# Performance work log

Hardware: AMD Instinct MI355X
Metric: run time of the kernel (lower is better)

## Reference

```python
import math
import jax, jax.numpy as jnp
import numpy as np

N_EMBD = 768
N_HEAD = 12
BLOCK_SIZE = 1024
B, T, N_ENC = 8, 1024, 257
EPS = 1e-5


def _ln(x, g, b):
    m = jnp.mean(x, axis=-1, keepdims=True)
    v = jnp.var(x, axis=-1, keepdims=True)
    return (x - m) * jax.lax.rsqrt(v + EPS) * g + b


def _heads(t, n_head):
    B_, N_, C_ = t.shape
    return t.reshape(B_, N_, n_head, C_ // n_head).transpose(0, 2, 1, 3)  # [B,H,N,D]


def setup_inputs() -> dict:
    key = jax.random.key(0)
    ks = jax.random.split(key, 16)
    s = 0.02
    d, h4, dq = N_EMBD, 4 * N_EMBD, N_EMBD // 4
    inp = {
        'x': jax.random.normal(ks[0], (B, T, d), jnp.float32),
        'x_enc': jax.random.normal(ks[1], (B, N_ENC, d), jnp.float32),
        'ln1_g': jnp.ones((d,), jnp.float32), 'ln1_b': jnp.zeros((d,), jnp.float32),
        'ln2_g': jnp.ones((d,), jnp.float32), 'ln2_b': jnp.zeros((d,), jnp.float32),
        'ln3_g': jnp.ones((d,), jnp.float32), 'ln3_b': jnp.zeros((d,), jnp.float32),
        'attn_w': jax.random.normal(ks[2], (d, 3 * d), jnp.float32) * s,
        'attn_bias': jnp.zeros((3 * d,), jnp.float32),
        'attn_proj_w': jax.random.normal(ks[3], (d, d), jnp.float32) * s,
        'attn_proj_b': jnp.zeros((d,), jnp.float32),
        'img_w': jax.random.normal(ks[4], (d, 2 * d), jnp.float32) * s,
        'img_b': jnp.zeros((2 * d,), jnp.float32),
        'cap_w': jax.random.normal(ks[5], (d, d), jnp.float32) * s,
        'cap_b': jnp.zeros((d,), jnp.float32),
        'cross_proj_w': jax.random.normal(ks[6], (d, d), jnp.float32) * s,
        'cross_proj_b': jnp.zeros((d,), jnp.float32),
        'ad1_w': jax.random.normal(ks[7], (d, dq), jnp.float32) * s,
        'ad1_b': jnp.zeros((dq,), jnp.float32),
        'ad2_w': jax.random.normal(ks[8], (dq, d), jnp.float32) * s,
        'ad2_b': jnp.zeros((d,), jnp.float32),
        'fc_w': jax.random.normal(ks[9], (d, h4), jnp.float32) * s,
        'fc_b': jnp.zeros((h4,), jnp.float32),
        'mproj_w': jax.random.normal(ks[10], (h4, d), jnp.float32) * s,
        'mproj_b': jnp.zeros((d,), jnp.float32),
    }
    return inp


def _block(x, x_enc, ln1_g, ln1_b, ln2_g, ln2_b, ln3_g, ln3_b,
           attn_w, attn_bias, attn_proj_w, attn_proj_b,
           img_w, img_b, cap_w, cap_b, cross_proj_w, cross_proj_b,
           ad1_w, ad1_b, ad2_w, ad2_b, fc_w, fc_b, mproj_w, mproj_b):
    d, nh = N_EMBD, N_HEAD
    hd = d // nh
    scale = 1.0 / math.sqrt(hd)

    def adapter(h):
        return jax.nn.relu(h @ ad1_w + ad1_b) @ ad2_w + ad2_b

    # --- causal self-attention ---
    h = _ln(x, ln1_g, ln1_b)
    qkv = h @ attn_w + attn_bias
    q, k, v = jnp.split(qkv, 3, axis=2)
    q, k, v = _heads(q, nh), _heads(k, nh), _heads(v, nh)  # [B,H,T,hd]
    att = jnp.einsum('bhqd,bhkd->bhqk', q, k) * scale
    Tq = x.shape[1]
    causal = jnp.tril(jnp.ones((Tq, Tq), bool))
    att = jnp.where(causal, att, -jnp.inf)
    att = jax.nn.softmax(att, axis=-1)
    sa = jnp.einsum('bhqk,bhkd->bhqd', att, v).transpose(0, 2, 1, 3).reshape(x.shape)
    sa = sa @ attn_proj_w + attn_proj_b
    x = x + adapter(sa)

    # --- cross-attention (queries from x, keys/values from x_enc) ---
    hq = _ln(x, ln1_g, ln1_b)
    he = _ln(x_enc, ln3_g, ln3_b)
    kv = he @ img_w + img_b
    k2, v2 = jnp.split(kv, 2, axis=2)
    q2 = hq @ cap_w + cap_b
    q2, k2, v2 = _heads(q2, nh), _heads(k2, nh), _heads(v2, nh)
    catt = jax.nn.softmax(jnp.einsum('bhqd,bhkd->bhqk', q2, k2) * scale, axis=-1)
    ca = jnp.einsum('bhqk,bhkd->bhqd', catt, v2).transpose(0, 2, 1, 3).reshape(x.shape)
    ca = ca @ cross_proj_w + cross_proj_b
    x = x + adapter(ca)

    # --- MLP ---
    hm = _ln(x, ln2_g, ln2_b)
    m = jax.nn.gelu(hm @ fc_w + fc_b, approximate=True) @ mproj_w + mproj_b
    x = x + adapter(m)
    return x, x_enc


def reference(x, x_enc, ln1_g, ln1_b, ln2_g, ln2_b, ln3_g, ln3_b,
              attn_w, attn_bias, attn_proj_w, attn_proj_b,
              img_w, img_b, cap_w, cap_b, cross_proj_w, cross_proj_b,
              ad1_w, ad1_b, ad2_w, ad2_b, fc_w, fc_b, mproj_w, mproj_b):
    return _block(x, x_enc, ln1_g, ln1_b, ln2_g, ln2_b, ln3_g, ln3_b,
                  attn_w, attn_bias, attn_proj_w, attn_proj_b,
                  img_w, img_b, cap_w, cap_b, cross_proj_w, cross_proj_b,
                  ad1_w, ad1_b, ad2_w, ad2_b, fc_w, fc_b, mproj_w, mproj_b)
```

## Files before the change

### kernel.cpp

```cpp
#include <hip/hip_runtime.h>

typedef unsigned short u16;
typedef short bf16x8 __attribute__((ext_vector_type(8)));
typedef float f32x4 __attribute__((ext_vector_type(4)));
typedef unsigned short u16x4 __attribute__((ext_vector_type(4)));

__device__ __forceinline__ u16 f2bf(float f) {
  union { float f; unsigned u; } v; v.f = f;
  unsigned u = v.u;
  unsigned r = (u + 0x7FFFu + ((u >> 16) & 1u)) >> 16;
  return (u16)r;
}
__device__ __forceinline__ float bf2f(u16 h) {
  union { unsigned u; float f; } v; v.u = ((unsigned)h) << 16;
  return v.f;
}
__device__ __forceinline__ unsigned cvt_pk_bf16(float lo, float hi) {
  unsigned d;
  asm("v_cvt_pk_bf16_f32 %0, %1, %2" : "=v"(d) : "v"(lo), "v"(hi));
  return d;
}
__device__ __forceinline__ float gelu_f(float x) {
  const float c1 = -2.302585093f;
  const float c2 = -0.1029620967f;
  float t = __builtin_fmaf(x * x, c2, c1) * x;
  float e = exp2f(t);
  return x * __builtin_amdgcn_rcpf(e + 1.0f);
}

#define GLD_LDS16(gp, lp)                                             \
  __builtin_amdgcn_global_load_lds(                                   \
      (const __attribute__((address_space(1))) void*)(gp),            \
      (__attribute__((address_space(3))) void*)(lp), 16, 0, 0)

template<int OFF>
__device__ __forceinline__ u16x4 tr16(unsigned a) {
  u16x4 d;
  asm volatile("ds_read_b64_tr_b16 %0, %1 offset:%2" : "=&v"(d) : "v"(a), "n"(OFF));
  return d;
}
__device__ __forceinline__ bf16x8 pack8(u16x4 a, u16x4 b) {
  union { u16x4 p[2]; bf16x8 v; } u;
  u.p[0] = a; u.p[1] = b;
  return u.v;
}
__device__ __forceinline__ u16x4 pack4(unsigned w0, unsigned w1) {
  union { unsigned w[2]; u16x4 v; } u;
  u.w[0] = w0; u.w[1] = w1;
  return u.v;
}

struct TrBatch {
  const float* W[9];
  u16* Bt[9];
  int K[9], N[9], Kpad[9], Npad[9];
  int tstart[10];
};
__global__ __launch_bounds__(256)
void transpose_all(TrBatch tb) {
  __shared__ float tile[64][65];
  const int tid = blockIdx.x;
  int mi = 0;
  while (mi < 8 && tid >= tb.tstart[mi + 1]) ++mi;
  const int lt = tid - tb.tstart[mi];
  const int tx = tb.Npad[mi] >> 6;
  const int n0 = (lt % tx) * 64;
  const int k0 = (lt / tx) * 64;
  const float* W = tb.W[mi];
  u16* Bt = tb.Bt[mi];
  const int K = tb.K[mi], N = tb.N[mi], Kpad = tb.Kpad[mi];
  const int t = threadIdx.x;
  const int c = t & 63;
  const int rb = t >> 6;
#pragma unroll
  for (int i = 0; i < 16; ++i) {
    int r = i * 4 + rb;
    float v = 0.f;
    if (k0 + r < K && n0 + c < N) v = W[(size_t)(k0 + r) * N + n0 + c];
    tile[r][c] = v;
  }
  __syncthreads();
#pragma unroll
  for (int i = 0; i < 16; ++i) {
    int r = i * 4 + rb;
    Bt[(size_t)(n0 + r) * Kpad + k0 + c] = f2bf(tile[c][r]);
  }
}

__global__ __launch_bounds__(64)
void ln_kernel(const float* __restrict__ X, const float* __restrict__ G,
               const float* __restrict__ Bv, u16* __restrict__ O, int Mreal) {
  const int row = blockIdx.x;
  const int l = threadIdx.x;
  u16* op = O + (size_t)row * 768;
  if (row >= Mreal) {
    u16x4 z = {0, 0, 0, 0};
#pragma unroll
    for (int i = 0; i < 3; ++i) *(u16x4*)(op + (i * 64 + l) * 4) = z;
    return;
  }
  const float* xp = X + (size_t)row * 768;
  float v[12];
  float s = 0.f, s2 = 0.f;
#pragma unroll
  for (int i = 0; i < 3; ++i) {
    float4 t4 = *(const float4*)(xp + (i * 64 + l) * 4);
    v[i * 4 + 0] = t4.x; v[i * 4 + 1] = t4.y; v[i * 4 + 2] = t4.z; v[i * 4 + 3] = t4.w;
    s += t4.x + t4.y + t4.z + t4.w;
    s2 += t4.x * t4.x + t4.y * t4.y + t4.z * t4.z + t4.w * t4.w;
  }
#pragma unroll
  for (int off = 32; off > 0; off >>= 1) {
    s += __shfl_xor(s, off);
    s2 += __shfl_xor(s2, off);
  }
  const float mean = s * (1.0f / 768.0f);
  const float var = s2 * (1.0f / 768.0f) - mean * mean;
  const float rstd = rsqrtf(var + 1e-5f);
#pragma unroll
  for (int i = 0; i < 3; ++i) {
    int base = (i * 64 + l) * 4;
    float4 g4 = *(const float4*)(G + base);
    float4 b4 = *(const float4*)(Bv + base);
    u16x4 o4;
    o4[0] = f2bf((v[i * 4 + 0] - mean) * rstd * g4.x + b4.x);
    o4[1] = f2bf((v[i * 4 + 1] - mean) * rstd * g4.y + b4.y);
    o4[2] = f2bf((v[i * 4 + 2] - mean) * rstd * g4.z + b4.z);
    o4[3] = f2bf((v[i * 4 + 3] - mean) * rstd * g4.w + b4.w);
    *(u16x4*)(op + base) = o4;
  }
}

template<bool DOLN, bool RESID>
__global__ __launch_bounds__(64)
void resid_ln(const float* __restrict__ S, float* __restrict__ D,
              const u16* __restrict__ P,
              const float* __restrict__ G, const float* __restrict__ Bv,
              u16* __restrict__ O) {
  const int row = blockIdx.x;
  const int l = threadIdx.x;
  const float* sp = S + (size_t)row * 768;
  float* dp = D + (size_t)row * 768;
  float v[12];
  float s = 0.f, s2 = 0.f;
#pragma unroll
  for (int i = 0; i < 3; ++i) {
    const int base = (i * 64 + l) * 4;
    float4 t4 = *(const float4*)(sp + base);
    if (RESID) {
      u16x4 p4 = *(const u16x4*)(P + (size_t)row * 768 + base);
      t4.x += bf2f(p4[0]); t4.y += bf2f(p4[1]);
      t4.z += bf2f(p4[2]); t4.w += bf2f(p4[3]);
    }
    v[i * 4 + 0] = t4.x; v[i * 4 + 1] = t4.y; v[i * 4 + 2] = t4.z; v[i * 4 + 3] = t4.w;
    s += t4.x + t4.y + t4.z + t4.w;
    s2 += t4.x * t4.x + t4.y * t4.y + t4.z * t4.z + t4.w * t4.w;
    *(float4*)(dp + base) = t4;
  }
  if (DOLN) {
#pragma unroll
    for (int off = 32; off > 0; off >>= 1) {
      s += __shfl_xor(s, off);
      s2 += __shfl_xor(s2, off);
    }
    const float mean = s * (1.0f / 768.0f);
    const float var = s2 * (1.0f / 768.0f) - mean * mean;
    const float rstd = rsqrtf(var + 1e-5f);
    u16* op = O + (size_t)row * 768;
#pragma unroll
    for (int i = 0; i < 3; ++i) {
      int base = (i * 64 + l) * 4;
      float4 g4 = *(const float4*)(G + base);
      float4 b4 = *(const float4*)(Bv + base);
      u16x4 o4;
      o4[0] = f2bf((v[i * 4 + 0] - mean) * rstd * g4.x + b4.x);
      o4[1] = f2bf((v[i * 4 + 1] - mean) * rstd * g4.y + b4.y);
      o4[2] = f2bf((v[i * 4 + 2] - mean) * rstd * g4.z + b4.z);
      o4[3] = f2bf((v[i * 4 + 3] - mean) * rstd * g4.w + b4.w);
      *(u16x4*)(op + base) = o4;
    }
  }
}

template<int MODE>
__global__ void gemm_bt(const u16* __restrict__ A, const u16* __restrict__ Bt,
                        void* __restrict__ C, const float* __restrict__ bias,
                        int K, int ldc, int nbias) {
  __shared__ u16 As[2 * 128 * 32];
  __shared__ u16 Bs[2 * 128 * 32];
  const int t = threadIdx.x;
  const int lane = t & 63;
  const int wid = t >> 6;
  const int wm = (wid >> 1) * 64;
  const int wn = (wid & 1) * 64;
  const int tm = blockIdx.x * 128;
  const int tn = blockIdx.y * 128;

  f32x4 zero = {0.f, 0.f, 0.f, 0.f};
  f32x4 acc[4][4];
#pragma unroll
  for (int i = 0; i < 4; ++i)
#pragma unroll
    for (int j = 0; j < 4; ++j) acc[i][j] = zero;

  const int rowA = lane & 15;
  const int kb = (((lane >> 4) ^ ((rowA >> 1) & 3)) << 3);
  const int kTiles = K >> 6;
  for (int kt = 0; kt < kTiles; ++kt) {
    const int kk = kt << 6;
#pragma unroll
    for (int i = 0; i < 4; ++i) {
      const int c = i * 256 + t;
      const int r = (c >> 2) & 127;
      const int cc = ((c >> 9) << 5) + ((((c & 3) ^ ((r >> 1) & 3))) << 3);
      GLD_LDS16(A + (size_t)(tm + r) * K + kk + cc, As + c * 8);
      GLD_LDS16(Bt + (size_t)(tn + r) * K + kk + cc, Bs + c * 8);
    }
    __syncthreads();
#pragma unroll
    for (int ks = 0; ks < 2; ++ks) {
      bf16x8 af[4], bfr[4];
      const int base = ks * 4096;
#pragma unroll
      for (int i = 0; i < 4; ++i) {
        af[i] = *(const bf16x8*)(As + base + (wm + i * 16 + rowA) * 32 + kb);
        bfr[i] = *(const bf16x8*)(Bs + base + (wn + i * 16 + rowA) * 32 + kb);
      }
#pragma unroll
      for (int mi = 0; mi < 4; ++mi)
#pragma unroll
        for (int ni = 0; ni < 4; ++ni)
          acc[mi][ni] = __builtin_amdgcn_mfma_f32_16x16x32_bf16(af[mi], bfr[ni], acc[mi][ni], 0, 0, 0);
    }
    __syncthreads();
  }
  const int col0 = lane & 15;
  const int row0 = (lane >> 4) << 2;
#pragma unroll
  for (int mi = 0; mi < 4; ++mi) {
#pragma unroll
    for (int ni = 0; ni < 4; ++ni) {
      int col = tn + wn + ni * 16 + col0;
      float bb = (col < nbias) ? bias[col] : 0.f;
      float vv[4];
#pragma unroll
      for (int r = 0; r < 4; ++r) {
        float v = acc[mi][ni][r] + bb;
        if (MODE == 1) v = fmaxf(v, 0.f);
        else if (MODE == 2) v = gelu_f(v);
        vv[r] = v;
      }
      unsigned w0 = cvt_pk_bf16(vv[0], vv[1]);
      unsigned w1 = cvt_pk_bf16(vv[2], vv[3]);
      size_t row = (size_t)(tm + wm + mi * 16 + row0);
      u16* cp = (u16*)C + row * ldc + col;
      cp[0] = (u16)w0;
      cp[(size_t)ldc] = (u16)(w0 >> 16);
      cp[(size_t)ldc * 2] = (u16)w1;
      cp[(size_t)ldc * 3] = (u16)(w1 >> 16);
    }
  }
}

struct GemmJob {
  const u16* A; const u16* Bt; u16* C; const float* bias;
  int K, ldc, nbias, mblocks;
};
__global__ __launch_bounds__(256)
void gemm_bt_dual(GemmJob j0, GemmJob j1, int split) {
  __shared__ u16 As[2 * 128 * 32];
  __shared__ u16 Bs[2 * 128 * 32];
  const int bid = blockIdx.x;
  const GemmJob& J = (bid < split) ? j0 : j1;
  const int lb = (bid < split) ? bid : bid - split;
  const int tm = (lb % J.mblocks) * 128;
  const int tn = (lb / J.mblocks) * 128;
  const u16* A = J.A;
  const u16* Bt = J.Bt;
  const int K = J.K;

  const int t = threadIdx.x;
  const int lane = t & 63;
  const int wid = t >> 6;
  const int wm = (wid >> 1) * 64;
  const int wn = (wid & 1) * 64;

  f32x4 zero = {0.f, 0.f, 0.f, 0.f};
  f32x4 acc[4][4];
#pragma unroll
  for (int i = 0; i < 4; ++i)
#pragma unroll
    for (int j = 0; j < 4; ++j) acc[i][j] = zero;

  const int rowA = lane & 15;
  const int kb = (((lane >> 4) ^ ((rowA >> 1) & 3)) << 3);
  const int kTiles = K >> 6;
  for (int kt = 0; kt < kTiles; ++kt) {
    const int kk = kt << 6;
#pragma unroll
    for (int i = 0; i < 4; ++i) {
      const int c = i * 256 + t;
      const int r = (c >> 2) & 127;
      const int cc = ((c >> 9) << 5) + ((((c & 3) ^ ((r >> 1) & 3))) << 3);
      GLD_LDS16(A + (size_t)(tm + r) * K + kk + cc, As + c * 8);
      GLD_LDS16(Bt + (size_t)(tn + r) * K + kk + cc, Bs + c * 8);
    }
    __syncthreads();
#pragma unroll
    for (int ks = 0; ks < 2; ++ks) {
      bf16x8 af[4], bfr[4];
      const int base = ks * 4096;
#pragma unroll
      for (int i = 0; i < 4; ++i) {
        af[i] = *(const bf16x8*)(As + base + (wm + i * 16 + rowA) * 32 + kb);
        bfr[i] = *(const bf16x8*)(Bs + base + (wn + i * 16 + rowA) * 32 + kb);
      }
#pragma unroll
      for (int mi = 0; mi < 4; ++mi)
#pragma unroll
        for (int ni = 0; ni < 4; ++ni)
          acc[mi][ni] = __builtin_amdgcn_mfma_f32_16x16x32_bf16(af[mi], bfr[ni], acc[mi][ni], 0, 0, 0);
    }
    __syncthreads();
  }
  const int col0 = lane & 15;
  const int row0 = (lane >> 4) << 2;
#pragma unroll
  for (int mi = 0; mi < 4; ++mi) {
#pragma unroll
    for (int ni = 0; ni < 4; ++ni) {
      int col = tn + wn + ni * 16 + col0;
      float bb = (col < J.nbias) ? J.bias[col] : 0.f;
      unsigned w0 = cvt_pk_bf16(acc[mi][ni][0] + bb, acc[mi][ni][1] + bb);
      unsigned w1 = cvt_pk_bf16(acc[mi][ni][2] + bb, acc[mi][ni][3] + bb);
      size_t row = (size_t)(tm + wm + mi * 16 + row0);
      u16* cp = J.C + row * J.ldc + col;
      cp[0] = (u16)w0;
      cp[(size_t)J.ldc] = (u16)(w0 >> 16);
      cp[(size_t)J.ldc * 2] = (u16)w1;
      cp[(size_t)J.ldc * 3] = (u16)(w1 >> 16);
    }
  }
}

template<bool CAUSAL>
__global__ __launch_bounds__(256)
void attn_mfma(const u16* __restrict__ Q, const u16* __restrict__ Kp,
               const u16* __restrict__ Vp,
               u16* __restrict__ O0, u16* __restrict__ O1, float2* __restrict__ ML,
               int seqkv, int qrs, int krs,
               long long qBatch, long long kBatch,
               int qoff, int koff, int voff) {
  __shared__ __align__(16) u16 Ks[64 * 64];
  __shared__ __align__(16) u16 Vs[4096];
  __shared__ __align__(16) u16 Ps[4][1024];
  const int t = threadIdx.x;
  const int lane = t & 63;
  const int wid = t >> 6;
  const int b = blockIdx.x / 12, h = blockIdx.x % 12;
  const int yq = CAUSAL ? ((int)gridDim.y - 1 - (int)blockIdx.y) : (int)blockIdx.y;
  const int q0 = yq * 64;
  const int colid = lane & 15;
  const int rgrp = lane >> 4;
  const int z = CAUSAL ? blockIdx.z : 0;

  int kt_begin = 0, kt_end;
  if (CAUSAL) {
    const int ntr = yq + 1;
    const int half = (ntr + 1) >> 1;
    kt_begin = z ? half : 0;
    kt_end = z ? ntr : half;
  } else {
    kt_end = (seqkv + 63) >> 6;
  }
  u16* Op = (CAUSAL && z) ? O1 : O0;

  if (CAUSAL && kt_begin >= kt_end) {
    if (colid == 0) {
#pragma unroll
      for (int r = 0; r < 4; ++r) {
        int qrow = q0 + wid * 16 + rgrp * 4 + r;
        ML[((size_t)z * 8192 + b * 1024 + qrow) * 12 + h] = make_float2(-1e30f, 0.f);
      }
    }
    return;
  }

  const u16* qp = Q + (size_t)b * qBatch + qoff + (size_t)(q0 + wid * 16 + colid) * qrs + h * 64;
  bf16x8 qa[2];
#pragma unroll
  for (int s = 0; s < 2; ++s) qa[s] = *(const bf16x8*)(qp + s * 32 + (rgrp << 3));

  f32x4 oacc[4];
#pragma unroll
  for (int i = 0; i < 4; ++i) oacc[i] = (f32x4){0.f, 0.f, 0.f, 0.f};
  float m[4] = {-1e30f, -1e30f, -1e30f, -1e30f};
  float l[4] = {0.f, 0.f, 0.f, 0.f};

  const u16* kbase = Kp + (size_t)b * kBatch + koff + h * 64;
  const u16* vbase = Vp + (size_t)b * kBatch + voff + h * 64;

  const int srr = t >> 3, sdc = t & 7;
  int kwo[2], vwo[2];
#pragma unroll
  for (int i = 0; i < 2; ++i) {
    const int r = srr + 32 * i;
    kwo[i] = r * 64 + ((sdc ^ (r & 7)) << 3);
    vwo[i] = ((sdc >> 1) << 10) + (i << 9) + (((srr >> 2) & 1) << 8)
           + (((srr >> 3) & 3) << 6) + ((srr & 3) << 4) + (((2 * sdc) & 3) << 2);
  }
  const unsigned vs_base = (unsigned)(size_t)&Vs[0] + 8u * (unsigned)lane;
  const unsigned ps_base = (unsigned)(size_t)&Ps[wid][0] + 8u * (unsigned)lane;

  bf16x8 kz[2], vz[2];
  auto LOADT = [&](int kt) {
    const int k0 = kt * 64;
#pragma unroll
    for (int i = 0; i < 2; ++i) {
      const int tk = k0 + srr + 32 * i;
      const int dc = sdc << 3;
      kz[i] = (bf16x8){0, 0, 0, 0, 0, 0, 0, 0};
      vz[i] = (bf16x8){0, 0, 0, 0, 0, 0, 0, 0};
      if (tk < seqkv) {
        kz[i] = *(const bf16x8*)(kbase + (size_t)tk * krs + dc);
        vz[i] = *(const bf16x8*)(vbase + (size_t)tk * krs + dc);
      }
    }
  };
  LOADT(kt_begin);

  constexpr float SC2 = 0.18033688011112042f;

  for (int kt = kt_begin; kt < kt_end; ++kt) {
    const int k0 = kt * 64;
#pragma unroll
    for (int i = 0; i < 2; ++i) {
      *(bf16x8*)&Ks[kwo[i]] = kz[i];
      *(bf16x8*)&Vs[vwo[i]] = vz[i];
    }
    __syncthreads();
    if (kt + 1 < kt_end) LOADT(kt + 1);

    f32x4 sacc[4];
#pragma unroll
    for (int c = 0; c < 4; ++c) sacc[c] = (f32x4){0.f, 0.f, 0.f, 0.f};
#pragma unroll
    for (int c = 0; c < 4; ++c)
#pragma unroll
      for (int s = 0; s < 2; ++s) {
        bf16x8 kf = *(const bf16x8*)&Ks[(c * 16 + colid) * 64 +
                                        ((((s << 2) + rgrp) ^ (colid & 7)) << 3)];
        sacc[c] = __builtin_amdgcn_mfma_f32_16x16x32_bf16(qa[s], kf, sacc[c], 0, 0, 0);
      }

    const bool domask = CAUSAL ? (kt == yq) : (kt == kt_end - 1);
    if (domask) {
#pragma unroll
      for (int c = 0; c < 4; ++c) {
        int kv = k0 + c * 16 + colid;
#pragma unroll
        for (int r = 0; r < 4; ++r) {
          int q = q0 + wid * 16 + rgrp * 4 + r;
          if ((CAUSAL && kv > q) || (!CAUSAL && kv >= seqkv)) sacc[c][r] = -1e30f;
        }
      }
    }

    float pms[4];
#pragma unroll
    for (int r = 0; r < 4; ++r) {
      float v = fmaxf(fmaxf(sacc[0][r], sacc[1][r]), fmaxf(sacc[2][r], sacc[3][r]));
#pragma unroll
      for (int off = 1; off < 16; off <<= 1) v = fmaxf(v, __shfl_xor(v, off));
      pms[r] = v * SC2;
    }
    bool ok = (pms[0] <= m[0] + 8.f) && (pms[1] <= m[1] + 8.f) &&
              (pms[2] <= m[2] + 8.f) && (pms[3] <= m[3] + 8.f);
    if (!__all(ok)) {
#pragma unroll
      for (int r = 0; r < 4; ++r) {
        float newm = fmaxf(m[r], pms[r]);
        float corr = exp2f(m[r] - newm);
        m[r] = newm;
        l[r] *= corr;
#pragma unroll
        for (int dc2 = 0; dc2 < 4; ++dc2) oacc[dc2][r] *= corr;
      }
    }

    float pv[4][4];
    float psum[4] = {0.f, 0.f, 0.f, 0.f};
#pragma unroll
    for (int c = 0; c < 4; ++c)
#pragma unroll
      for (int r = 0; r < 4; ++r) {
        float p = exp2f(__builtin_fmaf(sacc[c][r], SC2, -m[r]));
        pv[c][r] = p;
        psum[r] += p;
      }
#pragma unroll
    for (int r = 0; r < 4; ++r) {
#pragma unroll
      for (int off = 1; off < 16; off <<= 1) psum[r] += __shfl_xor(psum[r], off);
      l[r] += psum[r];
    }

#pragma unroll
    for (int c = 0; c < 4; ++c) {
      unsigned w0 = cvt_pk_bf16(pv[c][0], pv[c][1]);
      unsigned w1 = cvt_pk_bf16(pv[c][2], pv[c][3]);
      const int pa = ((c >> 1) << 9) + (((colid >> 2) & 1) << 8)
                   + (((2 * c + (colid >> 3)) & 3) << 6) + ((colid & 3) << 4) + (rgrp << 2);
      *(u16x4*)&Ps[wid][pa] = pack4(w0, w1);
    }
    __builtin_amdgcn_sched_barrier(0);

    u16x4 p00 = tr16<0>(ps_base);
    u16x4 p01 = tr16<512>(ps_base);
    u16x4 p10 = tr16<1024>(ps_base);
    u16x4 p11 = tr16<1536>(ps_base);
    asm volatile("s_waitcnt lgkmcnt(0)" ::: "memory");
    __builtin_amdgcn_sched_barrier(0);
    bf16x8 pf0 = pack8(p00, p01);
    bf16x8 pf1 = pack8(p10, p11);

#pragma unroll
    for (int dc2 = 0; dc2 < 4; ++dc2) {
      const unsigned va = vs_base + (unsigned)(dc2 * 2048);
      u16x4 v00 = tr16<0>(va);
      u16x4 v01 = tr16<512>(va);
      u16x4 v10 = tr16<1024>(va);
      u16x4 v11 = tr16<1536>(va);
      asm volatile("s_waitcnt lgkmcnt(0)" ::: "memory");
      __builtin_amdgcn_sched_barrier(0);
      bf16x8 vf0 = pack8(v00, v01);
      bf16x8 vf1 = pack8(v10, v11);
      oacc[dc2] = __builtin_amdgcn_mfma_f32_16x16x32_bf16(pf0, vf0, oacc[dc2], 0, 0, 0);
      oacc[dc2] = __builtin_amdgcn_mfma_f32_16x16x32_bf16(pf1, vf1, oacc[dc2], 0, 0, 0);
    }
    __syncthreads();
  }

#pragma unroll
  for (int r = 0; r < 4; ++r) {
    int qrow = q0 + wid * 16 + rgrp * 4 + r;
    u16* op = Op + ((size_t)b * 1024 + qrow) * 768 + h * 64;
    if (CAUSAL) {
      unsigned w0 = cvt_pk_bf16(oacc[0][r], oacc[1][r]);
      unsigned w1 = cvt_pk_bf16(oacc[2][r], oacc[3][r]);
      op[colid] = (u16)w0;
      op[16 + colid] = (u16)(w0 >> 16);
      op[32 + colid] = (u16)w1;
      op[48 + colid] = (u16)(w1 >> 16);
      if (colid == 0)
        ML[((size_t)z * 8192 + b * 1024 + qrow) * 12 + h] = make_float2(m[r], l[r]);
    } else {
      float inv = 1.f / l[r];
      unsigned w0 = cvt_pk_bf16(oacc[0][r] * inv, oacc[1][r] * inv);
      unsigned w1 = cvt_pk_bf16(oacc[2][r] * inv, oacc[3][r] * inv);
      op[colid] = (u16)w0;
      op[16 + colid] = (u16)(w0 >> 16);
      op[32 + colid] = (u16)w1;
      op[48 + colid] = (u16)(w1 >> 16);
    }
  }
}

__global__ __launch_bounds__(64)
void attn_combine(const u16* __restrict__ P0, const u16* __restrict__ P1,
                  const float2* __restrict__ ML, u16* __restrict__ O) {
  const int row = blockIdx.x;
  const int l = threadIdx.x;
#pragma unroll
  for (int i = 0; i < 3; ++i) {
    const int base = (i * 64 + l) * 4;
    const int h = base >> 6;
    float2 ml0 = ML[(size_t)row * 12 + h];
    float2 ml1 = ML[(size_t)8192 * 12 + row * 12 + h];
    float mm = fmaxf(ml0.x, ml1.x);
    float w0 = exp2f(ml0.x - mm);
    float w1 = exp2f(ml1.x - mm);
    float inv = 1.f / (ml0.y * w0 + ml1.y * w1);
    u16x4 a = *(const u16x4*)(P0 + (size_t)row * 768 + base);
    u16x4 c = *(const u16x4*)(P1 + (size_t)row * 768 + base);
    u16x4 o4;
#pragma unroll
    for (int j = 0; j < 4; ++j)
      o4[j] = f2bf((bf2f(a[j]) * w0 + bf2f(c[j]) * w1) * inv);
    *(u16x4*)(O + (size_t)row * 768 + base) = o4;
  }
}

extern "C" void kernel_launch(void* const* d_in, const int* in_sizes, int n_in,
                              void* d_out, int out_size, void* d_ws, size_t ws_size,
                              hipStream_t stream) {
  const float* x        = (const float*)d_in[0];
  const float* x_enc    = (const float*)d_in[1];
  const float* ln1_g    = (const float*)d_in[2];
  const float* ln1_b    = (const float*)d_in[3];
  const float* ln2_g    = (const float*)d_in[4];
  const float* ln2_b    = (const float*)d_in[5];
  const float* ln3_g    = (const float*)d_in[6];
  const float* ln3_b    = (const float*)d_in[7];
  const float* attn_w   = (const float*)d_in[8];
  const float* attn_bias= (const float*)d_in[9];
  const float* proj_w   = (const float*)d_in[10];
  const float* proj_b   = (const float*)d_in[11];
  const float* img_w    = (const float*)d_in[12];
  const float* img_b    = (const float*)d_in[13];
  const float* cap_w    = (const float*)d_in[14];
  const float* cap_b    = (const float*)d_in[15];
  const float* cross_w  = (const float*)d_in[16];
  const float* cross_b  = (const float*)d_in[17];
  const float* ad1_w    = (const float*)d_in[18];
  const float* ad1_b    = (const float*)d_in[19];
  const float* ad2_w    = (const float*)d_in[20];
  const float* ad2_b    = (const float*)d_in[21];
  const float* fc_w     = (const float*)d_in[22];
  const float* fc_b     = (const float*)d_in[23];
  const float* mproj_w  = (const float*)d_in[24];
  const float* mproj_b  = (const float*)d_in[25];

  const int Mx = 8192;
  const int Me = 2056;
  const int MeP = 2176;

  float* out_x  = (float*)d_out;
  float* out_xe = out_x + (size_t)Mx * 768;

  char* ws = (char*)d_ws;
  size_t off = 0;
  auto alloc = [&](size_t elems) {
    u16* p = (u16*)(ws + off);
    off = (off + elems * 2 + 255) & ~(size_t)255;
    return p;
  };
  u16* wt_attn  = alloc((size_t)2304 * 768);
  u16* wt_proj  = alloc((size_t)768 * 768);
  u16* wt_img   = alloc((size_t)1536 * 768);
  u16* wt_cap   = alloc((size_t)768 * 768);
  u16* wt_cross = alloc((size_t)768 * 768);
  u16* wt_ad1   = alloc((size_t)256 * 768);
  u16* wt_ad2   = alloc((size_t)768 * 256);
  u16* wt_fc    = alloc((size_t)3072 * 768);
  u16* wt_mproj = alloc((size_t)768 * 3072);
  u16* hbuf     = alloc((size_t)Mx * 768);
  u16* big      = alloc((size_t)Mx * 3072);
  u16* p0       = alloc((size_t)Mx * 768);
  u16* p1       = alloc((size_t)Mx * 768);
  u16* hid      = alloc((size_t)Mx * 256);
  float2* mlbuf = (float2*)alloc((size_t)2 * 8192 * 12 * 4);
  u16* q2  = big;
  u16* kvb = big + (size_t)Mx * 768;

  hipMemcpyAsync(out_xe, x_enc, (size_t)Me * 768 * 4, hipMemcpyDeviceToDevice, stream);

  TrBatch tb;
  int nt = 0;
  tb.tstart[0] = 0;
  auto addT = [&](const float* W, u16* Bt, int K, int N, int Kp, int Np) {
    tb.W[nt] = W; tb.Bt[nt] = Bt; tb.K[nt] = K; tb.N[nt] = N;
    tb.Kpad[nt] = Kp; tb.Npad[nt] = Np;
    tb.tstart[nt + 1] = tb.tstart[nt] + (Np / 64) * (Kp / 64);
    ++nt;
  };
  addT(attn_w, wt_attn, 768, 2304, 768, 2304);
  addT(proj_w, wt_proj, 768, 768, 768, 768);
  addT(img_w, wt_img, 768, 1536, 768, 1536);
  addT(cap_w, wt_cap, 768, 768, 768, 768);
  addT(cross_w, wt_cross, 768, 768, 768, 768);
  addT(ad1_w, wt_ad1, 768, 192, 768, 256);
  addT(ad2_w, wt_ad2, 192, 768, 256, 768);
  addT(fc_w, wt_fc, 768, 3072, 768, 3072);
  addT(mproj_w, wt_mproj, 3072, 768, 3072, 768);
  transpose_all<<<tb.tstart[9], 256, 0, stream>>>(tb);

  auto GEMM = [&](const u16* A, const u16* Bt, void* C, const float* bias,
                  int M, int N, int K, int ldc, int nbias, int mode) {
    dim3 g(M / 128, N / 128);
    if (mode == 0)      gemm_bt<0><<<g, 256, 0, stream>>>(A, Bt, C, bias, K, ldc, nbias);
    else if (mode == 1) gemm_bt<1><<<g, 256, 0, stream>>>(A, Bt, C, bias, K, ldc, nbias);
    else                gemm_bt<2><<<g, 256, 0, stream>>>(A, Bt, C, bias, K, ldc, nbias);
  };
  auto ADAPTER = [&](const u16* in, u16* padw) {
    GEMM(in, wt_ad1, hid, ad1_b, Mx, 256, 768, 256, 192, 1);
    GEMM(hid, wt_ad2, padw, ad2_b, Mx, 768, 256, 768, 768, 0);
  };

  resid_ln<true, false><<<Mx, 64, 0, stream>>>(x, out_x, nullptr, ln1_g, ln1_b, hbuf);

  GEMM(hbuf, wt_attn, big, attn_bias, Mx, 2304, 768, 2304, 2304, 0);
  attn_mfma<true><<<dim3(96, 16, 2), 256, 0, stream>>>(
      big, big, big, hbuf, p1, mlbuf, 1024, 2304, 2304,
      (long long)1024 * 2304, (long long)1024 * 2304, 0, 768, 1536);
  attn_combine<<<Mx, 64, 0, stream>>>(hbuf, p1, mlbuf, p0);
  GEMM(p0, wt_proj, p1, proj_b, Mx, 768, 768, 768, 768, 0);
  ADAPTER(p1, p0);
  resid_ln<true, true><<<Mx, 64, 0, stream>>>(out_x, out_x, p0, ln1_g, ln1_b, hbuf);

  ln_kernel<<<MeP, 64, 0, stream>>>(x_enc, ln3_g, ln3_b, p0, Me);
  {
    GemmJob jkv = { p0,   wt_img, kvb, img_b, 768, 1536, 1536, MeP / 128 };
    GemmJob jq2 = { hbuf, wt_cap, q2,  cap_b, 768, 768,  768,  Mx / 128 };
    const int split = (MeP / 128) * (1536 / 128);
    const int total = split + (Mx / 128) * (768 / 128);
    gemm_bt_dual<<<total, 256, 0, stream>>>(jkv, jq2, split);
  }
  attn_mfma<false><<<dim3(96, 16), 256, 0, stream>>>(
      q2, kvb, kvb, p1, nullptr, nullptr, 257, 768, 1536,
      (long long)1024 * 768, (long long)257 * 1536, 0, 0, 768);
  GEMM(p1, wt_cross, p0, cross_b, Mx, 768, 768, 768, 768, 0);
  ADAPTER(p0, p1);
  resid_ln<true, true><<<Mx, 64, 0, stream>>>(out_x, out_x, p1, ln2_g, ln2_b, hbuf);

  GEMM(hbuf, wt_fc, big, fc_b, Mx, 3072, 768, 3072, 3072, 2);
  GEMM(big, wt_mproj, p0, mproj_b, Mx, 768, 3072, 768, 768, 0);
  ADAPTER(p0, p1);
  resid_ln<false, true><<<Mx, 64, 0, stream>>>(out_x, out_x, p1, nullptr, nullptr, nullptr);

  (void)in_sizes; (void)n_in; (void)out_size; (void)ws_size;
}
```

Baseline: 469.2 us.

## Add intra-block split-K GEMM with two K halves reduced through LDS

Adds a 512-thread GEMM variant in which two groups of four waves each process half of the K range into separate LDS buffers. The second half's partial accumulators are then summed into the first through shared memory before the epilogue. It replaces the standard GEMM for the N=768 projections, the mproj GEMM and the first adapter GEMM, which launch relatively few 128x128 tiles. The aim is more waves in flight and better latency hiding for these narrow GEMMs, at the cost of more LDS, an extra reduction pass and higher register pressure per block.

```diff
diff --git a/kernel.cpp b/kernel.cpp
--- a/kernel.cpp
+++ b/kernel.cpp
@@ -234,6 +234,110 @@
     }
     __syncthreads();
   }
+  const int col0 = lane & 15;
+  const int row0 = (lane >> 4) << 2;
+#pragma unroll
+  for (int mi = 0; mi < 4; ++mi) {
+#pragma unroll
+    for (int ni = 0; ni < 4; ++ni) {
+      int col = tn + wn + ni * 16 + col0;
+      float bb = (col < nbias) ? bias[col] : 0.f;
+      float vv[4];
+#pragma unroll
+      for (int r = 0; r < 4; ++r) {
+        float v = acc[mi][ni][r] + bb;
+        if (MODE == 1) v = fmaxf(v, 0.f);
+        else if (MODE == 2) v = gelu_f(v);
+        vv[r] = v;
+      }
+      unsigned w0 = cvt_pk_bf16(vv[0], vv[1]);
+      unsigned w1 = cvt_pk_bf16(vv[2], vv[3]);
+      size_t row = (size_t)(tm + wm + mi * 16 + row0);
+      u16* cp = (u16*)C + row * ldc + col;
+      cp[0] = (u16)w0;
+      cp[(size_t)ldc] = (u16)(w0 >> 16);
+      cp[(size_t)ldc * 2] = (u16)w1;
+      cp[(size_t)ldc * 3] = (u16)(w1 >> 16);
+    }
+  }
+}
+
+template<int MODE>
+__global__ __launch_bounds__(512)
+void gemm_bt_sk8(const u16* __restrict__ A, const u16* __restrict__ Bt,
+                 void* __restrict__ C, const float* __restrict__ bias,
+                 int K, int ldc, int nbias) {
+  __shared__ __align__(16) u16 As[2][2 * 128 * 32];
+  __shared__ __align__(16) u16 Bs[2][2 * 128 * 32];
+  const int t = threadIdx.x;
+  const int tl = t & 255;
+  const int half = t >> 8;
+  const int lane = t & 63;
+  const int w4 = (t >> 6) & 3;
+  const int wm = (w4 >> 1) * 64;
+  const int wn = (w4 & 1) * 64;
+  const int tm = blockIdx.x * 128;
+  const int tn = blockIdx.y * 128;
+
+  f32x4 zero = {0.f, 0.f, 0.f, 0.f};
+  f32x4 acc[4][4];
+#pragma unroll
+  for (int i = 0; i < 4; ++i)
+#pragma unroll
+    for (int j = 0; j < 4; ++j) acc[i][j] = zero;
+
+  const int rowA = lane & 15;
+  const int kb = (((lane >> 4) ^ ((rowA >> 1) & 3)) << 3);
+  const int kh = (K >> 6) >> 1;
+  const int k0t = half * kh;
+
+  for (int kt = 0; kt < kh; ++kt) {
+    const int kk = (k0t + kt) << 6;
+#pragma unroll
+    for (int i = 0; i < 4; ++i) {
+      const int c = i * 256 + tl;
+      const int r = (c >> 2) & 127;
+      const int cc = ((c >> 9) << 5) + ((((c & 3) ^ ((r >> 1) & 3))) << 3);
+      GLD_LDS16(A + (size_t)(tm + r) * K + kk + cc, &As[half][c * 8]);
+      GLD_LDS16(Bt + (size_t)(tn + r) * K + kk + cc, &Bs[half][c * 8]);
+    }
+    __syncthreads();
+#pragma unroll
+    for (int ks = 0; ks < 2; ++ks) {
+      bf16x8 af[4], bfr[4];
+      const int base = ks * 4096;
+#pragma unroll
+      for (int i = 0; i < 4; ++i) {
+        af[i] = *(const bf16x8*)(&As[half][base + (wm + i * 16 + rowA) * 32 + kb]);
+        bfr[i] = *(const bf16x8*)(&Bs[half][base + (wn + i * 16 + rowA) * 32 + kb]);
+      }
+#pragma unroll
+      for (int mi = 0; mi < 4; ++mi)
+#pragma unroll
+        for (int ni = 0; ni < 4; ++ni)
+          acc[mi][ni] = __builtin_amdgcn_mfma_f32_16x16x32_bf16(af[mi], bfr[ni], acc[mi][ni], 0, 0, 0);
+    }
+    __syncthreads();
+  }
+
+  float* red = ((w4 & 2) ? (float*)&Bs[0][0] : (float*)&As[0][0]) + (w4 & 1) * 4096;
+  if (half) {
+#pragma unroll
+    for (int mi = 0; mi < 4; ++mi)
+#pragma unroll
+      for (int ni = 0; ni < 4; ++ni)
+        *(f32x4*)&red[((mi * 4 + ni) << 8) + (lane << 2)] = acc[mi][ni];
+  }
+  __syncthreads();
+  if (half) return;
+#pragma unroll
+  for (int mi = 0; mi < 4; ++mi)
+#pragma unroll
+    for (int ni = 0; ni < 4; ++ni) {
+      f32x4 o = *(const f32x4*)&red[((mi * 4 + ni) << 8) + (lane << 2)];
+      acc[mi][ni] += o;
+    }
+
   const int col0 = lane & 15;
   const int row0 = (lane >> 4) << 2;
 #pragma unroll
@@ -682,8 +786,14 @@
     else if (mode == 1) gemm_bt<1><<<g, 256, 0, stream>>>(A, Bt, C, bias, K, ldc, nbias);
     else                gemm_bt<2><<<g, 256, 0, stream>>>(A, Bt, C, bias, K, ldc, nbias);
   };
+  auto GEMM_SK = [&](const u16* A, const u16* Bt, void* C, const float* bias,
+                     int M, int N, int K, int ldc, int nbias, int mode) {
+    dim3 g(M / 128, N / 128);
+    if (mode == 0) gemm_bt_sk8<0><<<g, 512, 0, stream>>>(A, Bt, C, bias, K, ldc, nbias);
+    else           gemm_bt_sk8<1><<<g, 512, 0, stream>>>(A, Bt, C, bias, K, ldc, nbias);
+  };
   auto ADAPTER = [&](const u16* in, u16* padw) {
-    GEMM(in, wt_ad1, hid, ad1_b, Mx, 256, 768, 256, 192, 1);
+    GEMM_SK(in, wt_ad1, hid, ad1_b, Mx, 256, 768, 256, 192, 1);
     GEMM(hid, wt_ad2, padw, ad2_b, Mx, 768, 256, 768, 768, 0);
   };
 
@@ -694,7 +804,7 @@
       big, big, big, hbuf, p1, mlbuf, 1024, 2304, 2304,
       (long long)1024 * 2304, (long long)1024 * 2304, 0, 768, 1536);
   attn_combine<<<Mx, 64, 0, stream>>>(hbuf, p1, mlbuf, p0);
-  GEMM(p0, wt_proj, p1, proj_b, Mx, 768, 768, 768, 768, 0);
+  GEMM_SK(p0, wt_proj, p1, proj_b, Mx, 768, 768, 768, 768, 0);
   ADAPTER(p1, p0);
   resid_ln<true, true><<<Mx, 64, 0, stream>>>(out_x, out_x, p0, ln1_g, ln1_b, hbuf);
 
@@ -709,12 +819,12 @@
   attn_mfma<false><<<dim3(96, 16), 256, 0, stream>>>(
       q2, kvb, kvb, p1, nullptr, nullptr, 257, 768, 1536,
       (long long)1024 * 768, (long long)257 * 1536, 0, 0, 768);
-  GEMM(p1, wt_cross, p0, cross_b, Mx, 768, 768, 768, 768, 0);
+  GEMM_SK(p1, wt_cross, p0, cross_b, Mx, 768, 768, 768, 768, 0);
   ADAPTER(p0, p1);
   resid_ln<true, true><<<Mx, 64, 0, stream>>>(out_x, out_x, p1, ln2_g, ln2_b, hbuf);
 
   GEMM(hbuf, wt_fc, big, fc_b, Mx, 3072, 768, 3072, 3072, 2);
-  GEMM(big, wt_mproj, p0, mproj_b, Mx, 768, 3072, 768, 768, 0);
+  GEMM_SK(big, wt_mproj, p0, mproj_b, Mx, 768, 3072, 768, 768, 0);
   ADAPTER(p0, p1);
   resid_ln<false, true><<<Mx, 64, 0, stream>>>(out_x, out_x, p1, nullptr, nullptr, nullptr);
 
```

New measurement: 521.9 us. 1.11x slower.
